# Performance work log

Hardware: AMD Instinct MI355X
Metric: run time of the kernel (lower is better)

The kernel has to match this reference:

```python
import jax, jax.numpy as jnp
import numpy as np

BLOCK = 16  # NVFP4 block size (one fp8e4m3 scale per 16 elements)
FP4_LEVELS = jnp.array([0.0, 0.5, 1.0, 1.5, 2.0, 3.0, 4.0, 6.0], dtype=jnp.float32)  # e2m1 magnitudes
FP4_MIDS = jnp.array([0.25, 0.75, 1.25, 1.75, 2.5, 3.5, 5.0], dtype=jnp.float32)     # round-to-nearest midpoints
FP8_MIN = 2.0 ** -9   # smallest positive fp8e4m3 subnormal (guards div-by-zero after scale cast)
FP8_MAX = 448.0


def fp8_e4m3_round(x):
    """Emulate casting positive float32 values to fp8 e4m3 (3 mantissa bits)."""
    e = jnp.clip(jnp.floor(jnp.log2(jnp.maximum(x, 1e-30))), -6.0, 8.0)  # -6 = min normal exponent
    step = jnp.exp2(e - 3.0)
    return jnp.clip(jnp.round(x / step) * step, 0.0, FP8_MAX)


def fp4_e2m1_quant(x):
    """Round-to-nearest onto the signed fp4 e2m1 grid {0,±0.5,±1,±1.5,±2,±3,±4,±6}."""
    idx = jnp.sum(jnp.abs(x)[..., None] > FP4_MIDS, axis=-1)
    return jnp.sign(x) * FP4_LEVELS[idx]


def quantize_activations(x2):
    """x2: [M, K] -> (fp4 values [M, K//16, 16], fp8 block scales [M, K//16])."""
    M, K = x2.shape
    xb = x2.reshape(M, K // BLOCK, BLOCK)
    amax = jnp.max(jnp.abs(xb), axis=-1)                      # per-16-block absmax
    s = jnp.maximum(fp8_e4m3_round(jnp.maximum(amax / 6.0, 1e-12)), FP8_MIN)
    q = fp4_e2m1_quant(xb / s[..., None])
    return q, s


def setup_inputs() -> dict:
    key = jax.random.key(0)
    k1, k2, k3 = jax.random.split(key, 3)
    in_f, out_f, tokens = 4096, 16384, 4096
    x = jax.random.normal(k1, (1, tokens, in_f), dtype=jnp.float32)
    # Build NVFP4 weights: quantize a random bf16-like weight per 16-element block.
    w = jax.random.normal(k2, (out_f, in_f), dtype=jnp.float32) * 0.02
    wb = w.reshape(out_f, in_f // BLOCK, BLOCK)
    weight_scale = jnp.maximum(fp8_e4m3_round(jnp.maximum(jnp.max(jnp.abs(wb), axis=-1) / 6.0, 1e-12)), FP8_MIN)
    weight_q = fp4_e2m1_quant(wb / weight_scale[..., None]).reshape(out_f, in_f)
    bias = jax.random.normal(k3, (out_f,), dtype=jnp.float32) * 0.01
    return {"x": x, "weight_q": weight_q, "weight_scale": weight_scale, "bias": bias}


def reference(x, weight_q, weight_scale, bias):
    orig_shape = x.shape
    K = orig_shape[-1]
    x2 = x.reshape(-1, K)                                     # [M, K]
    qa, sa = quantize_activations(x2)                          # fp4 values + fp8 block scales
    x_deq = (qa * sa[..., None]).reshape(x2.shape)             # dequantized activations
    N = weight_q.shape[0]
    w_deq = (weight_q.reshape(N, K // BLOCK, BLOCK) * weight_scale[..., None]).reshape(N, K)
    out = x2.dtype.type(0) + x_deq @ w_deq.T + bias[None, :]   # scaled_mm equivalent + bias
    return out.reshape(*orig_shape[:-1], N)
```

## Files before the change

### kernel.cpp

```cpp
#include <hip/hip_runtime.h>
#include <hip/hip_bf16.h>
#include <stdint.h>

typedef __attribute__((ext_vector_type(4))) float  f32x4;
typedef __attribute__((ext_vector_type(8))) short  bf16x8;
typedef __attribute__((ext_vector_type(8))) unsigned short u16x8;

#define MFMA16(d, x, y) d = __builtin_amdgcn_mfma_f32_16x16x32_bf16(x, y, d, 0, 0, 0)

static __device__ inline unsigned short f2bf(float f) {
    union { float f; unsigned u; } a; a.f = f;
    unsigned u = a.u;
    unsigned lsb = (u >> 16) & 1u;
    u += 0x7fffu + lsb;
    return (unsigned short)(u >> 16);
}

static __device__ inline float fp8_e4m3_round(float x) {
    union { float f; unsigned u; } a; a.f = x;
    int e = (int)((a.u >> 23) & 255u) - 127;
    e = e < -6 ? -6 : (e > 8 ? 8 : e);
    union { unsigned u; float f; } stp, inv;
    stp.u = (unsigned)(e - 3 + 127) << 23;
    inv.u = (unsigned)(3 - e + 127) << 23;
    float r = rintf(x * inv.f) * stp.f;
    return fminf(r, 448.0f);
}

static __device__ inline float fp4_level(float a) {
    return a > 2.5f ? (a > 3.5f ? (a > 5.0f ? 6.0f : 4.0f) : 3.0f)
                    : (a > 1.25f ? (a > 1.75f ? 2.0f : 1.5f)
                                 : (a > 0.75f ? 1.0f : (a > 0.25f ? 0.5f : 0.0f)));
}

__global__ void pre_kernel(const float* __restrict__ x, unsigned short* __restrict__ xd, int nblkx,
                           const float* __restrict__ wq, const float* __restrict__ wsc,
                           unsigned short* __restrict__ wd, int nblkw) {
    int i = blockIdx.x * blockDim.x + threadIdx.x;
    if (i < nblkx) {
        const float4* p = (const float4*)(x + (size_t)i * 16);
        float4 v0 = p[0], v1 = p[1], v2 = p[2], v3 = p[3];
        float vals[16] = { v0.x,v0.y,v0.z,v0.w, v1.x,v1.y,v1.z,v1.w,
                           v2.x,v2.y,v2.z,v2.w, v3.x,v3.y,v3.z,v3.w };
        float amax = 0.0f;
#pragma unroll
        for (int j = 0; j < 16; ++j) amax = fmaxf(amax, fabsf(vals[j]));
        float s0 = fmaxf(amax / 6.0f, 1e-12f);
        float s  = fmaxf(fp8_e4m3_round(s0), 1.0f / 512.0f);
        u16x8 o0, o1;
#pragma unroll
        for (int j = 0; j < 16; ++j) {
            float v = vals[j] / s;
            float lev = fp4_level(fabsf(v));
            float q = copysignf(lev, v);
            unsigned short b = f2bf(q * s);
            if (j < 8) o0[j] = b; else o1[j - 8] = b;
        }
        u16x8* dst = (u16x8*)(xd + (size_t)i * 16);
        dst[0] = o0; dst[1] = o1;
    } else {
        int j = i - nblkx;
        if (j >= nblkw) return;
        float s = wsc[j];
        const float4* p = (const float4*)(wq + (size_t)j * 16);
        float4 v0 = p[0], v1 = p[1], v2 = p[2], v3 = p[3];
        float vals[16] = { v0.x,v0.y,v0.z,v0.w, v1.x,v1.y,v1.z,v1.w,
                           v2.x,v2.y,v2.z,v2.w, v3.x,v3.y,v3.z,v3.w };
        u16x8 o0, o1;
#pragma unroll
        for (int k = 0; k < 16; ++k) {
            unsigned short b = f2bf(vals[k] * s);
            if (k < 8) o0[k] = b; else o1[k - 8] = b;
        }
        u16x8* dst = (u16x8*)(wd + (size_t)j * 16);
        dst[0] = o0; dst[1] = o1;
    }
}

static __device__ __forceinline__ void stage_half(const unsigned short* g0, const unsigned short* g1,
                                                  size_t koff, char* d0) {
    __builtin_amdgcn_global_load_lds((const __attribute__((address_space(1))) void*)(g0 + koff),
                                     (__attribute__((address_space(3))) void*)d0, 16, 0, 0);
    __builtin_amdgcn_global_load_lds((const __attribute__((address_space(1))) void*)(g1 + koff),
                                     (__attribute__((address_space(3))) void*)(d0 + 1024), 16, 0, 0);
}

#define MFMA_ALL(AV, BV) {                                              \
    _Pragma("unroll")                                                   \
    for (int mf = 0; mf < 8; ++mf) {                                    \
        _Pragma("unroll")                                               \
        for (int nf = 0; nf < 4; ++nf) MFMA16(acc[mf][nf], AV[mf], BV[nf]); } }

#define READ12(AV, BV, OFF) {                                           \
    const char* _pa = lds + (OFF) + wr * 8192 + lane_off;               \
    const char* _pb = lds + 65536 + (OFF) + wc * 4096 + lane_off;       \
    _Pragma("unroll")                                                   \
    for (int i = 0; i < 8; ++i) AV[i] = *(const bf16x8*)(_pa + i * 1024); \
    _Pragma("unroll")                                                   \
    for (int i = 0; i < 4; ++i) BV[i] = *(const bf16x8*)(_pb + i * 1024); }

#define SGB_CHAIN {                                                     \
    __builtin_amdgcn_sched_group_barrier(0x020, 4, 0);                  \
    __builtin_amdgcn_sched_group_barrier(0x100, 3, 0);                  \
    __builtin_amdgcn_sched_group_barrier(0x008, 8, 0);                  \
    __builtin_amdgcn_sched_group_barrier(0x100, 3, 0);                  \
    __builtin_amdgcn_sched_group_barrier(0x008, 8, 0);                  \
    __builtin_amdgcn_sched_group_barrier(0x100, 3, 0);                  \
    __builtin_amdgcn_sched_group_barrier(0x008, 8, 0);                  \
    __builtin_amdgcn_sched_group_barrier(0x100, 3, 0);                  \
    __builtin_amdgcn_sched_group_barrier(0x008, 8, 0); }

#define PH1(T, B) {                                                     \
    asm volatile("s_waitcnt vmcnt(4)" ::: "memory");                    \
    __builtin_amdgcn_s_barrier();                                       \
    __builtin_amdgcn_s_setprio(1);                                      \
    stage_half(gA0, gA1, (size_t)((T) + 1) * 64 + 32, ldsA_w + (1 - (B)) * 32768 + 16384); \
    stage_half(gB0, gB1, (size_t)((T) + 1) * 64 + 32, ldsB_w + (1 - (B)) * 32768 + 16384); \
    READ12(a2, b2, (B) * 32768 + 16384);                                \
    MFMA_ALL(a1, b1);                                                   \
    SGB_CHAIN;                                                          \
    __builtin_amdgcn_s_setprio(0); }

#define PH2(T, B) {                                                     \
    asm volatile("s_waitcnt vmcnt(4)" ::: "memory");                    \
    __builtin_amdgcn_s_barrier();                                       \
    __builtin_amdgcn_s_setprio(1);                                      \
    stage_half(gA0, gA1, (size_t)((T) + 2) * 64, ldsA_w + (B) * 32768); \
    stage_half(gB0, gB1, (size_t)((T) + 2) * 64, ldsB_w + (B) * 32768); \
    READ12(a1, b1, (1 - (B)) * 32768);                                  \
    MFMA_ALL(a2, b2);                                                   \
    SGB_CHAIN;                                                          \
    __builtin_amdgcn_s_setprio(0); }

__global__ __launch_bounds__(512, 2)
void gemm_kernel(const unsigned short* __restrict__ A, const unsigned short* __restrict__ Bw,
                 const float* __restrict__ bias, float* __restrict__ C,
                 int M, int N, int K) {
    extern __shared__ char lds[];
    const int tid  = threadIdx.x;
    const int lane = tid & 63;
    const int wid  = tid >> 6;
    const int wr   = wid >> 2;
    const int wc   = wid & 3;

    const int NXB = N >> 8, NYB = M >> 8;
    int bid = blockIdx.x;
    int bx, by;
    if (NXB == 64 && NYB == 16) {
        int xcd = bid & 7, c = bid >> 3;
        bx = xcd * 8 + (c & 7);
        by = c >> 3;
    } else { bx = bid % NXB; by = bid / NXB; }

    const int NT = K >> 6;

    int w0 = (lane & 15) * 64 + ((lane >> 4) << 4);
    const int lane_off = w0 ^ (((w0 >> 9) & 1) << 5);
    const int u   = (lane * 16) ^ (lane & 32);
    const int r_l = u >> 6;
    const int c_l = (u & 63) >> 1;

    const unsigned short* gA0 = A  + (size_t)(by * 256 + wid * 32 + r_l) * K + c_l;
    const unsigned short* gA1 = gA0 + (size_t)16 * K;
    const unsigned short* gB0 = Bw + (size_t)(bx * 256 + wid * 32 + r_l) * K + c_l;
    const unsigned short* gB1 = gB0 + (size_t)16 * K;
    char* ldsA_w = lds + wid * 2048 + lane * 16;
    char* ldsB_w = lds + 65536 + wid * 2048 + lane * 16;

    f32x4 acc[8][4];
#pragma unroll
    for (int m = 0; m < 8; ++m)
#pragma unroll
        for (int n = 0; n < 4; ++n)
#pragma unroll
            for (int j = 0; j < 4; ++j) acc[m][n][j] = 0.0f;

    bf16x8 a1[8], a2[8], b1[4], b2[4];

    stage_half(gA0, gA1, 0,  ldsA_w);
    stage_half(gB0, gB1, 0,  ldsB_w);
    stage_half(gA0, gA1, 32, ldsA_w + 16384);
    stage_half(gB0, gB1, 32, ldsB_w + 16384);
    stage_half(gA0, gA1, 64, ldsA_w + 32768);
    stage_half(gB0, gB1, 64, ldsB_w + 32768);
    asm volatile("s_waitcnt vmcnt(8)" ::: "memory");
    __builtin_amdgcn_s_barrier();
    READ12(a1, b1, 0);

    for (int t = 0; t <= NT - 4; t += 2) {
        PH1(t, 0);  PH2(t, 0);
        PH1(t + 1, 1);  PH2(t + 1, 1);
    }

    PH1(NT - 2, 0);
    {
        asm volatile("s_waitcnt vmcnt(4)" ::: "memory");
        __builtin_amdgcn_s_barrier();
        READ12(a1, b1, 32768);
        MFMA_ALL(a2, b2);
    }
    {
        asm volatile("s_waitcnt vmcnt(0)" ::: "memory");
        __builtin_amdgcn_s_barrier();
        READ12(a2, b2, 32768 + 16384);
        MFMA_ALL(a1, b1);
        MFMA_ALL(a2, b2);
    }

    const int row0 = by * 256 + wr * 128;
    const int col0 = bx * 256 + wc * 64;
#pragma unroll
    for (int nf = 0; nf < 4; ++nf) {
        int col = col0 + nf * 16 + (lane & 15);
        float bv = bias[col];
#pragma unroll
        for (int mf = 0; mf < 8; ++mf) {
#pragma unroll
            for (int j = 0; j < 4; ++j) {
                int row = row0 + mf * 16 + ((lane >> 4) << 2) + j;
                C[(size_t)row * N + col] = acc[mf][nf][j] + bv;
            }
        }
    }
}

extern "C" void kernel_launch(void* const* d_in, const int* in_sizes, int n_in,
                              void* d_out, int out_size, void* d_ws, size_t ws_size,
                              hipStream_t stream) {
    const float* x    = (const float*)d_in[0];
    const float* wq   = (const float*)d_in[1];
    const float* wsc  = (const float*)d_in[2];
    const float* bias = (const float*)d_in[3];
    float* out = (float*)d_out;

    const long N = in_sizes[3];
    const long K = (long)in_sizes[1] / N;
    const long M = (long)in_sizes[0] / K;

    size_t need = ((size_t)(M * K) + (size_t)(N * K)) * sizeof(unsigned short);
    if (ws_size < need) return;

    unsigned short* xd = (unsigned short*)d_ws;
    unsigned short* wd = xd + (size_t)M * K;

    {
        int nblkx = (int)(M * K / 16);
        int nblkw = (int)(N * K / 16);
        int total = nblkx + nblkw;
        pre_kernel<<<(total + 255) / 256, 256, 0, stream>>>(x, xd, nblkx, wq, wsc, wd, nblkw);
    }
    {
        hipFuncSetAttribute((const void*)gemm_kernel,
                            hipFuncAttributeMaxDynamicSharedMemorySize, 131072);
        int nwg = (int)((M / 256) * (N / 256));
        gemm_kernel<<<dim3(nwg), dim3(512), 131072, stream>>>(xd, wd, bias, out,
                                                              (int)M, (int)N, (int)K);
    }
}
```

Measured before the change: 668.3 us.

## Load B fragments directly from global into registers, bypass LDS for weights

Weight (B) tiles are no longer staged through LDS. Each wave now loads its own B fragments straight from global memory into registers with inline global_load_dwordx4, and LDS is halved to hold only A. This removes B's LDS write/read traffic and the sched_group_barrier interleave, and also changes the workgroup-to-tile mapping inside each XCD. The cost is uncoalesced, redundant global loads of B across waves sharing a column (the two wr rows both load the same B), plus coarser vmcnt waits that may expose memory latency before the MFMAs.

```diff
diff --git a/kernel.cpp b/kernel.cpp
--- a/kernel.cpp
+++ b/kernel.cpp
@@ -91,45 +91,42 @@
         _Pragma("unroll")                                               \
         for (int nf = 0; nf < 4; ++nf) MFMA16(acc[mf][nf], AV[mf], BV[nf]); } }
 
-#define READ12(AV, BV, OFF) {                                           \
+#define READ8A(AV, OFF) {                                               \
     const char* _pa = lds + (OFF) + wr * 8192 + lane_off;               \
-    const char* _pb = lds + 65536 + (OFF) + wc * 4096 + lane_off;       \
     _Pragma("unroll")                                                   \
-    for (int i = 0; i < 8; ++i) AV[i] = *(const bf16x8*)(_pa + i * 1024); \
+    for (int i = 0; i < 8; ++i) AV[i] = *(const bf16x8*)(_pa + i * 1024); }
+
+#define BLOAD4(DST, KOFF) {                                             \
     _Pragma("unroll")                                                   \
-    for (int i = 0; i < 4; ++i) BV[i] = *(const bf16x8*)(_pb + i * 1024); }
-
-#define SGB_CHAIN {                                                     \
-    __builtin_amdgcn_sched_group_barrier(0x020, 4, 0);                  \
-    __builtin_amdgcn_sched_group_barrier(0x100, 3, 0);                  \
-    __builtin_amdgcn_sched_group_barrier(0x008, 8, 0);                  \
-    __builtin_amdgcn_sched_group_barrier(0x100, 3, 0);                  \
-    __builtin_amdgcn_sched_group_barrier(0x008, 8, 0);                  \
-    __builtin_amdgcn_sched_group_barrier(0x100, 3, 0);                  \
-    __builtin_amdgcn_sched_group_barrier(0x008, 8, 0);                  \
-    __builtin_amdgcn_sched_group_barrier(0x100, 3, 0);                  \
-    __builtin_amdgcn_sched_group_barrier(0x008, 8, 0); }
+    for (int nf = 0; nf < 4; ++nf) {                                    \
+        const unsigned short* _p = gBr + (size_t)nf * 16 * K + (KOFF);  \
+        asm volatile("global_load_dwordx4 %0, %1, off"                  \
+                     : "=v"(DST[nf]) : "v"(_p)); } }
+
+#define VMW(N) asm volatile("s_waitcnt vmcnt(" #N ")" ::: "memory")
 
 #define PH1(T, B) {                                                     \
-    asm volatile("s_waitcnt vmcnt(4)" ::: "memory");                    \
+    VMW(10);                                                            \
     __builtin_amdgcn_s_barrier();                                       \
     __builtin_amdgcn_s_setprio(1);                                      \
     stage_half(gA0, gA1, (size_t)((T) + 1) * 64 + 32, ldsA_w + (1 - (B)) * 32768 + 16384); \
-    stage_half(gB0, gB1, (size_t)((T) + 1) * 64 + 32, ldsB_w + (1 - (B)) * 32768 + 16384); \
-    READ12(a2, b2, (B) * 32768 + 16384);                                \
+    BLOAD4(b2, (size_t)(T) * 64 + 32);                                  \
+    READ8A(a2, (B) * 32768 + 16384);                                    \
+    VMW(6);                                                             \
+    __builtin_amdgcn_sched_barrier(0);                                  \
     MFMA_ALL(a1, b1);                                                   \
-    SGB_CHAIN;                                                          \
     __builtin_amdgcn_s_setprio(0); }
 
 #define PH2(T, B) {                                                     \
-    asm volatile("s_waitcnt vmcnt(4)" ::: "memory");                    \
+    VMW(10);                                                            \
     __builtin_amdgcn_s_barrier();                                       \
     __builtin_amdgcn_s_setprio(1);                                      \
     stage_half(gA0, gA1, (size_t)((T) + 2) * 64, ldsA_w + (B) * 32768); \
-    stage_half(gB0, gB1, (size_t)((T) + 2) * 64, ldsB_w + (B) * 32768); \
-    READ12(a1, b1, (1 - (B)) * 32768);                                  \
+    BLOAD4(b1, (size_t)((T) + 1) * 64);                                 \
+    READ8A(a1, (1 - (B)) * 32768);                                      \
+    VMW(6);                                                             \
+    __builtin_amdgcn_sched_barrier(0);                                  \
     MFMA_ALL(a2, b2);                                                   \
-    SGB_CHAIN;                                                          \
     __builtin_amdgcn_s_setprio(0); }
 
 __global__ __launch_bounds__(512, 2)
@@ -148,8 +145,8 @@
     int bx, by;
     if (NXB == 64 && NYB == 16) {
         int xcd = bid & 7, c = bid >> 3;
-        bx = xcd * 8 + (c & 7);
-        by = c >> 3;
+        bx = xcd * 8 + (c >> 4);
+        by = c & 15;
     } else { bx = bid % NXB; by = bid / NXB; }
 
     const int NT = K >> 6;
@@ -160,12 +157,12 @@
     const int r_l = u >> 6;
     const int c_l = (u & 63) >> 1;
 
-    const unsigned short* gA0 = A  + (size_t)(by * 256 + wid * 32 + r_l) * K + c_l;
+    const unsigned short* gA0 = A + (size_t)(by * 256 + wid * 32 + r_l) * K + c_l;
     const unsigned short* gA1 = gA0 + (size_t)16 * K;
-    const unsigned short* gB0 = Bw + (size_t)(bx * 256 + wid * 32 + r_l) * K + c_l;
-    const unsigned short* gB1 = gB0 + (size_t)16 * K;
     char* ldsA_w = lds + wid * 2048 + lane * 16;
-    char* ldsB_w = lds + 65536 + wid * 2048 + lane * 16;
+
+    const unsigned short* gBr = Bw + (size_t)(bx * 256 + wc * 64 + (lane & 15)) * K
+                                   + ((lane >> 4) << 3);
 
     f32x4 acc[8][4];
 #pragma unroll
@@ -178,14 +175,12 @@
     bf16x8 a1[8], a2[8], b1[4], b2[4];
 
     stage_half(gA0, gA1, 0,  ldsA_w);
-    stage_half(gB0, gB1, 0,  ldsB_w);
     stage_half(gA0, gA1, 32, ldsA_w + 16384);
-    stage_half(gB0, gB1, 32, ldsB_w + 16384);
     stage_half(gA0, gA1, 64, ldsA_w + 32768);
-    stage_half(gB0, gB1, 64, ldsB_w + 32768);
-    asm volatile("s_waitcnt vmcnt(8)" ::: "memory");
+    BLOAD4(b1, 0);
+    VMW(8);
     __builtin_amdgcn_s_barrier();
-    READ12(a1, b1, 0);
+    READ8A(a1, 0);
 
     for (int t = 0; t <= NT - 4; t += 2) {
         PH1(t, 0);  PH2(t, 0);
@@ -194,16 +189,24 @@
 
     PH1(NT - 2, 0);
     {
-        asm volatile("s_waitcnt vmcnt(4)" ::: "memory");
+        VMW(10);
         __builtin_amdgcn_s_barrier();
-        READ12(a1, b1, 32768);
+        BLOAD4(b1, (size_t)(NT - 1) * 64);
+        READ8A(a1, 32768);
+        VMW(4);
+        __builtin_amdgcn_sched_barrier(0);
         MFMA_ALL(a2, b2);
     }
     {
-        asm volatile("s_waitcnt vmcnt(0)" ::: "memory");
+        VMW(8);
         __builtin_amdgcn_s_barrier();
-        READ12(a2, b2, 32768 + 16384);
+        BLOAD4(b2, (size_t)(NT - 1) * 64 + 32);
+        READ8A(a2, 32768 + 16384);
+        VMW(4);
+        __builtin_amdgcn_sched_barrier(0);
         MFMA_ALL(a1, b1);
+        VMW(0);
+        __builtin_amdgcn_sched_barrier(0);
         MFMA_ALL(a2, b2);
     }
 
@@ -251,9 +254,9 @@
     }
     {
         hipFuncSetAttribute((const void*)gemm_kernel,
-                            hipFuncAttributeMaxDynamicSharedMemorySize, 131072);
+                            hipFuncAttributeMaxDynamicSharedMemorySize, 65536);
         int nwg = (int)((M / 256) * (N / 256));
-        gemm_kernel<<<dim3(nwg), dim3(512), 131072, stream>>>(xd, wd, bias, out,
-                                                              (int)M, (int)N, (int)K);
-    }
-}
+        gemm_kernel<<<dim3(nwg), dim3(512), 65536, stream>>>(xd, wd, bias, out,
+                                                             (int)M, (int)N, (int)K);
+    }
+}
```

New measurement: 1.163 ms. +74.0%, slower.
